# Kernel optimization log

Hardware: AMD Instinct MI355X
Metric: run time of the kernel (lower is better)

Reference implementation:

```python
import jax, jax.numpy as jnp
import numpy as np

N = 50000      # nodes
E = 800000     # edges
D_IN = 128
D_H = 128
D_OUT = 64
P = 0.3        # dropout prob


def _glorot(key, out_c, in_c):
    return jax.random.normal(key, (out_c, in_c), jnp.float32) * (1.0 / np.sqrt(in_c))


def setup_inputs() -> dict:
    key = jax.random.key(0)
    ks = jax.random.split(key, 10)
    return {
        "x": jax.random.normal(ks[0], (N, D_IN), jnp.float32),
        "u1": jax.random.uniform(ks[1], (N, D_H), jnp.float32),
        "u2": jax.random.uniform(ks[2], (N, D_H), jnp.float32),
        "wl0": _glorot(ks[3], D_H, D_IN), "bl0": jnp.zeros((D_H,), jnp.float32), "wr0": _glorot(ks[4], D_H, D_IN),
        "wl1": _glorot(ks[5], D_H, D_H), "bl1": jnp.zeros((D_H,), jnp.float32), "wr1": _glorot(ks[6], D_H, D_H),
        "wl2": _glorot(ks[7], D_OUT, D_H), "bl2": jnp.zeros((D_OUT,), jnp.float32), "wr2": _glorot(ks[8], D_OUT, D_H),
        "edge_index": jax.random.randint(ks[9], (2, E), 0, N),
    }


def _sage_conv(x, src, dst, wl, bl, wr):
    # PyG SAGEConv (aggr='mean'): lin_l(mean of neighbor msgs) + lin_r(x)
    msg = x[src]                                                    # [E, d] gather
    s = jax.ops.segment_sum(msg, dst, num_segments=N)               # [N, d] scatter-sum
    cnt = jax.ops.segment_sum(jnp.ones((dst.shape[0],), x.dtype), dst, num_segments=N)
    mean = s / jnp.maximum(cnt, 1.0)[:, None]                       # mean; 0 for isolated nodes
    return mean @ wl.T + bl + x @ wr.T


def reference(x, u1, u2, wl0, bl0, wr0, wl1, bl1, wr1, wl2, bl2, wr2, edge_index):
    src, dst = edge_index[0], edge_index[1]
    keep = 1.0 - P
    h = jax.nn.relu(_sage_conv(x, src, dst, wl0, bl0, wr0))
    h = h * ((u1 >= P).astype(h.dtype) / keep)                      # dropout (training=True)
    h = jax.nn.relu(_sage_conv(h, src, dst, wl1, bl1, wr1))
    h = h * ((u2 >= P).astype(h.dtype) / keep)
    return _sage_conv(h, src, dst, wl2, bl2, wr2)
```

## Files before the change

### kernel.cpp

```cpp
#include <hip/hip_runtime.h>


constexpr int N = 50000;
constexpr int E = 800000;
constexpr int NBUCK = (N + 255) / 256;
constexpr int CE = 2048;
constexpr int NEB = (E + CE - 1) / CE;
constexpr int SLOT = 5632;
static_assert(N <= 65536, "u16 packing");

typedef _Float16 f16x8 __attribute__((ext_vector_type(8)));
typedef _Float16 f16x4 __attribute__((ext_vector_type(4)));
typedef _Float16 f16x2 __attribute__((ext_vector_type(2)));
typedef float f32x4 __attribute__((ext_vector_type(4)));


__global__ __launch_bounds__(256) void bucket_scatter_kernel(
    const int* __restrict__ src, const int* __restrict__ dst,
    int* __restrict__ bcur, unsigned* __restrict__ T) {
  __shared__ unsigned sorted[CE];
  __shared__ int hist[256], scan[256], excl[256], lcur[256], gbase[256];
  const int t = threadIdx.x;
  const int e0 = blockIdx.x * CE;
  const int nval = min(CE, E - e0);
  hist[t] = 0;
  __syncthreads();
  for (int i = t; i < nval; i += 256) atomicAdd(&hist[dst[e0 + i] >> 8], 1);
  __syncthreads();
  const int h = hist[t];
  scan[t] = h;
  __syncthreads();
  for (int off = 1; off < 256; off <<= 1) {
    int u = (t >= off) ? scan[t - off] : 0;
    __syncthreads();
    scan[t] += u;
    __syncthreads();
  }
  excl[t] = scan[t] - h;
  lcur[t] = scan[t] - h;
  gbase[t] = (t < NBUCK && h > 0) ? atomicAdd(&bcur[t], h) : 0;
  __syncthreads();
  for (int i = t; i < nval; i += 256) {
    int e = e0 + i;
    int d = dst[e];
    int p = atomicAdd(&lcur[d >> 8], 1);
    sorted[p] = ((unsigned)d << 16) | (unsigned)src[e];
  }
  __syncthreads();
  for (int i = t; i < nval; i += 256) {
    unsigned pk = sorted[i];
    int b = pk >> 24;
    T[gbase[b] + (i - excl[b])] = pk;
  }
}

__global__ __launch_bounds__(256) void bucket_place_kernel(
    const unsigned* __restrict__ T, const int* __restrict__ bcur,
    int* __restrict__ offs, int* __restrict__ deg, int* __restrict__ elist) {
  __shared__ int dcnt[256], s[256], ncur[256];
  const int t = threadIdx.x;
  const int b = blockIdx.x;
  const int lo = b * SLOT;
  const int hi = bcur[b];
  dcnt[t] = 0;
  __syncthreads();
  for (int i = lo + t; i < hi; i += 256) atomicAdd(&dcnt[(T[i] >> 16) & 255], 1);
  __syncthreads();
  const int v = dcnt[t];
  const int pv = (v + 3) & ~3;
  s[t] = pv;
  __syncthreads();
  for (int off = 1; off < 256; off <<= 1) {
    int u = (t >= off) ? s[t - off] : 0;
    __syncthreads();
    s[t] += u;
    __syncthreads();
  }
  const int base = lo + s[t] - pv;
  const int node = b * 256 + t;
  if (node < N) { offs[node] = base; deg[node] = v; }
  ncur[t] = base;
  __syncthreads();
  for (int i = lo + t; i < hi; i += 256) {
    unsigned pk = T[i];
    int pos = atomicAdd(&ncur[(pk >> 16) & 255], 1);
    elist[pos] = (int)(pk & 0xffffu);
  }
}

__device__ inline void wfrag_build(int idx, int KB, const float* wl,
                                   const float* wr, _Float16* wf) {
  int j = idx & 7;
  int lane = (idx >> 3) & 63;
  int kb = (idx >> 9) % KB;
  int ct = (idx >> 9) / KB;
  int c = ct * 16 + (lane & 15);
  int k = kb * 32 + (lane >> 4) * 8 + j;
  float v = (k < 128) ? wl[c * 128 + k] : wr[c * 128 + (k - 128)];
  wf[idx] = (_Float16)v;
}

constexpr int CONVB = (N * 128 / 8 + 255) / 256;
constexpr int MASKB = (N * 128) / (8 * 256);

__global__ __launch_bounds__(256) void setup_kernel(
    const float* __restrict__ x,
    const float* __restrict__ u1, const float* __restrict__ u2,
    const float* __restrict__ wl0, const float* __restrict__ wr0,
    const float* __restrict__ wl1, const float* __restrict__ wr1,
    const float* __restrict__ wl2, const float* __restrict__ wr2,
    _Float16* __restrict__ HA, _Float16* __restrict__ wf0,
    _Float16* __restrict__ wf1, _Float16* __restrict__ wfZ,
    unsigned* __restrict__ mk1, unsigned* __restrict__ mk2,
    int* __restrict__ bcur) {
  const int b = blockIdx.x;
  const int t = threadIdx.x;
  if (b < CONVB) {
    int i = b * 256 + t;
    if (i < N * 128 / 8) {
      float4 a = ((const float4*)x)[i * 2];
      float4 c = ((const float4*)x)[i * 2 + 1];
      f16x8 v;
      v[0] = (_Float16)a.x; v[1] = (_Float16)a.y; v[2] = (_Float16)a.z; v[3] = (_Float16)a.w;
      v[4] = (_Float16)c.x; v[5] = (_Float16)c.y; v[6] = (_Float16)c.z; v[7] = (_Float16)c.w;
      ((f16x8*)HA)[i] = v;
    }
  } else if (b < CONVB + 128) {
    wfrag_build((b - CONVB) * 256 + t, 8, wl0, wr0, wf0);
  } else if (b < CONVB + 256) {
    wfrag_build((b - CONVB - 128) * 256 + t, 8, wl1, wr1, wf1);
  } else if (b < CONVB + 320) {
    int idx = (b - CONVB - 256) * 256 + t;
    int j = idx & 7;
    int lane = (idx >> 3) & 63;
    int kb = (idx >> 9) & 3;
    int ct = idx >> 11;
    int c = ct * 16 + (lane & 15);
    int k = kb * 32 + (lane >> 4) * 8 + j;
    float v = (c < 64) ? wl2[c * 128 + k] : wr2[(c - 64) * 128 + k];
    wfZ[idx] = (_Float16)v;
  } else if (b < CONVB + 320 + 2 * MASKB) {
    int mb = b - (CONVB + 320);
    const float* Us = (mb < MASKB) ? u1 : u2;
    unsigned* MKs = (mb < MASKB) ? mk1 : mk2;
    int bb = (mb < MASKB) ? mb : (mb - MASKB);
#pragma unroll
    for (int k = 0; k < 8; ++k) {
      int i = (bb * 8 + k) * 256 + t;
      float uv = Us[i];
      unsigned long long m = __ballot(uv >= 0.3f);
      int lt = t & 63;
      if (lt == 0) MKs[i >> 5] = (unsigned)m;
      else if (lt == 32) MKs[i >> 5] = (unsigned)(m >> 32);
    }
  } else {
    if (t < NBUCK) bcur[t] = t * SLOT;
  }
}

__global__ __launch_bounds__(256, 4) void fused_layer_kernel(
    const _Float16* __restrict__ H, const int* __restrict__ offs,
    const int* __restrict__ deg, const int* __restrict__ elist,
    const _Float16* __restrict__ Wf, const float* __restrict__ bias,
    const unsigned* __restrict__ MK, _Float16* __restrict__ outp) {
  __shared__ __align__(16) _Float16 Af[2][8][64][8];
  const int t = threadIdx.x;
  const int rowbase = blockIdx.x * 32;

#pragma unroll
  for (int m2 = 0; m2 < 2; ++m2) {
    int m = t * 2 + m2;
    int r = m >> 4, o = m & 15;
    int row = min(rowbase + r, N - 1);
    f16x8 v = *(const f16x8*)(H + (size_t)row * 128 + o * 8);
    *(f16x8*)&Af[r >> 4][4 + (o >> 2)][(o & 3) * 16 + (r & 15)][0] = v;
  }

  {
    const int hw = t >> 5;
    const int ll = t & 31;
    const int kb = ll >> 3, q = (ll >> 1) & 3, j = (ll & 1) * 4;
#pragma unroll 1
    for (int i = 0; i < 4; ++i) {
      int r = hw * 4 + i;
      int node = rowbase + r;
      float a0 = 0.f, a1 = 0.f, a2 = 0.f, a3 = 0.f;
      int d = 0;
      if (node < N) {
        const int e0 = offs[node];
        d = deg[node];
        const int e1 = e0 + d;
        int e = e0;
        for (; e + 16 <= e1; e += 16) {
          int4 q0 = *(const int4*)(elist + e);
          int4 q1 = *(const int4*)(elist + e + 4);
          int4 q2 = *(const int4*)(elist + e + 8);
          int4 q3 = *(const int4*)(elist + e + 12);
          int s[16] = {q0.x, q0.y, q0.z, q0.w, q1.x, q1.y, q1.z, q1.w,
                       q2.x, q2.y, q2.z, q2.w, q3.x, q3.y, q3.z, q3.w};
          f16x4 v[16];
#pragma unroll
          for (int u = 0; u < 16; ++u)
            v[u] = *(const f16x4*)(H + (size_t)s[u] * 128 + ll * 4);
#pragma unroll
          for (int u = 0; u < 16; ++u) {
            a0 += (float)v[u][0]; a1 += (float)v[u][1];
            a2 += (float)v[u][2]; a3 += (float)v[u][3];
          }
        }
        for (; e + 4 <= e1; e += 4) {
          int4 qq4 = *(const int4*)(elist + e);
          int s[4] = {qq4.x, qq4.y, qq4.z, qq4.w};
          f16x4 v[4];
#pragma unroll
          for (int u = 0; u < 4; ++u)
            v[u] = *(const f16x4*)(H + (size_t)s[u] * 128 + ll * 4);
#pragma unroll
          for (int u = 0; u < 4; ++u) {
            a0 += (float)v[u][0]; a1 += (float)v[u][1];
            a2 += (float)v[u][2]; a3 += (float)v[u][3];
          }
        }
        for (; e < e1; ++e) {
          f16x4 v = *(const f16x4*)(H + (size_t)elist[e] * 128 + ll * 4);
          a0 += (float)v[0]; a1 += (float)v[1];
          a2 += (float)v[2]; a3 += (float)v[3];
        }
      }
      float inv = 1.0f / (float)max(d, 1);
      f16x4 o;
      o[0] = (_Float16)(a0 * inv); o[1] = (_Float16)(a1 * inv);
      o[2] = (_Float16)(a2 * inv); o[3] = (_Float16)(a3 * inv);
      *(f16x4*)&Af[r >> 4][kb][q * 16 + (r & 15)][j] = o;
    }
  }
  __syncthreads();

  const int lane = t & 63;
  const int w = t >> 6;
  const int n16 = lane & 15;
  const int qq = lane >> 4;
  const int colbase = w * 32;

  f32x4 acc[2][2];
#pragma unroll
  for (int h = 0; h < 2; ++h)
#pragma unroll
    for (int ct = 0; ct < 2; ++ct) acc[h][ct] = (f32x4){0.f, 0.f, 0.f, 0.f};

#pragma unroll
  for (int kb = 0; kb < 8; ++kb) {
    f16x8 a0 = *(const f16x8*)&Af[0][kb][lane][0];
    f16x8 a1 = *(const f16x8*)&Af[1][kb][lane][0];
#pragma unroll
    for (int ct = 0; ct < 2; ++ct) {
      const int ctg = w * 2 + ct;
      f16x8 b = *(const f16x8*)(Wf + ((size_t)(ctg * 8 + kb) * 64 + lane) * 8);
      acc[0][ct] = __builtin_amdgcn_mfma_f32_16x16x32_f16(a0, b, acc[0][ct], 0, 0, 0);
      acc[1][ct] = __builtin_amdgcn_mfma_f32_16x16x32_f16(a1, b, acc[1][ct], 0, 0, 0);
    }
  }

#pragma unroll
  for (int h = 0; h < 2; ++h) {
#pragma unroll
    for (int r = 0; r < 4; ++r) {
      int row = rowbase + h * 16 + qq * 4 + r;
      if (row < N) {
        unsigned mw = MK[(size_t)row * 4 + w];
#pragma unroll
        for (int ct = 0; ct < 2; ++ct) {
          const int col = colbase + ct * 16 + n16;
          float v = fmaxf(acc[h][ct][r] + bias[col], 0.f);
          v = ((mw >> (ct * 16 + n16)) & 1u) ? v * (1.0f / 0.7f) : 0.0f;
          outp[(size_t)row * 128 + col] = (_Float16)v;
        }
      }
    }
  }
}

__global__ __launch_bounds__(256) void gather64_add_kernel(
    const _Float16* __restrict__ Y2, const float* __restrict__ F,
    const int* __restrict__ offs, const int* __restrict__ deg,
    const int* __restrict__ elist, float* __restrict__ out) {
  int node = blockIdx.x * 8 + (threadIdx.x >> 5);
  if (node >= N) return;
  int l = threadIdx.x & 31;
  const int e0 = offs[node];
  const int d = deg[node];
  const int e1 = e0 + d;
  float a0 = 0.f, a1 = 0.f;
  int e = e0;
  for (; e + 16 <= e1; e += 16) {
    int4 q0 = *(const int4*)(elist + e);
    int4 q1 = *(const int4*)(elist + e + 4);
    int4 q2 = *(const int4*)(elist + e + 8);
    int4 q3 = *(const int4*)(elist + e + 12);
    int s[16] = {q0.x, q0.y, q0.z, q0.w, q1.x, q1.y, q1.z, q1.w,
                 q2.x, q2.y, q2.z, q2.w, q3.x, q3.y, q3.z, q3.w};
    f16x2 v[16];
#pragma unroll
    for (int u = 0; u < 16; ++u)
      v[u] = *(const f16x2*)(Y2 + (size_t)s[u] * 64 + l * 2);
#pragma unroll
    for (int u = 0; u < 16; ++u) { a0 += (float)v[u][0]; a1 += (float)v[u][1]; }
  }
  for (; e + 4 <= e1; e += 4) {
    int4 q = *(const int4*)(elist + e);
    int s[4] = {q.x, q.y, q.z, q.w};
    f16x2 v[4];
#pragma unroll
    for (int u = 0; u < 4; ++u)
      v[u] = *(const f16x2*)(Y2 + (size_t)s[u] * 64 + l * 2);
#pragma unroll
    for (int u = 0; u < 4; ++u) { a0 += (float)v[u][0]; a1 += (float)v[u][1]; }
  }
  for (; e < e1; ++e) {
    f16x2 v = *(const f16x2*)(Y2 + (size_t)elist[e] * 64 + l * 2);
    a0 += (float)v[0]; a1 += (float)v[1];
  }
  float inv = 1.0f / (float)max(d, 1);
  float2 f = ((const float2*)(F + (size_t)node * 64))[l];
  float2 o;
  o.x = f.x + a0 * inv;
  o.y = f.y + a1 * inv;
  ((float2*)(out + (size_t)node * 64))[l] = o;
}

__global__ __launch_bounds__(256, 4) void mfma_gemmZ_kernel(
    const _Float16* __restrict__ Hh, const _Float16* __restrict__ Wf,
    const float* __restrict__ bl2, _Float16* __restrict__ Y2,
    float* __restrict__ F) {
  const int lane = threadIdx.x & 63;
  const int w = threadIdx.x >> 6;
  const int n16 = lane & 15;
  const int q = lane >> 4;
  const int rowbase = blockIdx.x * 32;
  const int colbase = w * 32;

  f32x4 acc[2][2];
#pragma unroll
  for (int h = 0; h < 2; ++h)
#pragma unroll
    for (int ct = 0; ct < 2; ++ct) acc[h][ct] = (f32x4){0.f, 0.f, 0.f, 0.f};

  int ar0 = min(rowbase + n16, N - 1);
  int ar1 = min(rowbase + 16 + n16, N - 1);
  const _Float16* pH0 = Hh + (size_t)ar0 * 128 + q * 8;
  const _Float16* pH1 = Hh + (size_t)ar1 * 128 + q * 8;

#pragma unroll
  for (int kb = 0; kb < 4; ++kb) {
    const int ko = kb * 32;
    f16x8 a0 = *(const f16x8*)(pH0 + ko);
    f16x8 a1 = *(const f16x8*)(pH1 + ko);
#pragma unroll
    for (int ct = 0; ct < 2; ++ct) {
      const int ctg = w * 2 + ct;
      f16x8 b = *(const f16x8*)(Wf + ((size_t)(ctg * 4 + kb) * 64 + lane) * 8);
      acc[0][ct] = __builtin_amdgcn_mfma_f32_16x16x32_f16(a0, b, acc[0][ct], 0, 0, 0);
      acc[1][ct] = __builtin_amdgcn_mfma_f32_16x16x32_f16(a1, b, acc[1][ct], 0, 0, 0);
    }
  }

#pragma unroll
  for (int h = 0; h < 2; ++h) {
#pragma unroll
    for (int ct = 0; ct < 2; ++ct) {
      const int col = colbase + ct * 16 + n16;
#pragma unroll
      for (int r = 0; r < 4; ++r) {
        int row = rowbase + h * 16 + q * 4 + r;
        if (row < N) {
          float v = acc[h][ct][r];
          if (col < 64) Y2[(size_t)row * 64 + col] = (_Float16)v;
          else F[(size_t)row * 64 + (col - 64)] = v + bl2[col - 64];
        }
      }
    }
  }
}

extern "C" void kernel_launch(void* const* d_in, const int* in_sizes, int n_in,
                              void* d_out, int out_size, void* d_ws, size_t ws_size,
                              hipStream_t stream) {
  const float* x   = (const float*)d_in[0];
  const float* u1  = (const float*)d_in[1];
  const float* u2  = (const float*)d_in[2];
  const float* wl0 = (const float*)d_in[3];
  const float* bl0 = (const float*)d_in[4];
  const float* wr0 = (const float*)d_in[5];
  const float* wl1 = (const float*)d_in[6];
  const float* bl1 = (const float*)d_in[7];
  const float* wr1 = (const float*)d_in[8];
  const float* wl2 = (const float*)d_in[9];
  const float* bl2 = (const float*)d_in[10];
  const float* wr2 = (const float*)d_in[11];
  const int* edge  = (const int*)d_in[12];
  const int* src = edge;
  const int* dst = edge + E;

  _Float16* HA  = (_Float16*)d_ws;
  _Float16* HB  = HA + (size_t)N * 128;
  _Float16* M16 = HB + (size_t)N * 128;
  float* F      = (float*)(M16 + (size_t)N * 128);
  int* offs     = (int*)(F + (size_t)N * 64);
  int* deg      = offs + N;
  int* elist    = deg + N;
  unsigned* T   = (unsigned*)(elist + NBUCK * SLOT);
  int* bcur     = (int*)(T + NBUCK * SLOT);
  uintptr_t p = (uintptr_t)(bcur + NBUCK);
  p = (p + 15) & ~(uintptr_t)15;
  _Float16* wf0 = (_Float16*)p;
  _Float16* wf1 = wf0 + 8 * 8 * 512;
  _Float16* wfZ = wf1 + 8 * 8 * 512;
  unsigned* mk1 = (unsigned*)(wfZ + 8 * 4 * 512);
  unsigned* mk2 = mk1 + (size_t)N * 4;

  setup_kernel<<<CONVB + 320 + 2 * MASKB + 1, 256, 0, stream>>>(
      x, u1, u2, wl0, wr0, wl1, wr1, wl2, wr2, HA, wf0, wf1, wfZ, mk1, mk2,
      bcur);
  bucket_scatter_kernel<<<NEB, 256, 0, stream>>>(src, dst, bcur, T);
  bucket_place_kernel<<<NBUCK, 256, 0, stream>>>(T, bcur, offs, deg, elist);

  const int GM   = (N + 31) / 32;
  const int GG64 = (N + 7) / 8;

  fused_layer_kernel<<<GM, 256, 0, stream>>>(HA, offs, deg, elist, wf0, bl0, mk1, HB);
  fused_layer_kernel<<<GM, 256, 0, stream>>>(HB, offs, deg, elist, wf1, bl1, mk2, HA);
  mfma_gemmZ_kernel<<<GM, 256, 0, stream>>>(HA, wfZ, bl2, M16, F);
  gather64_add_kernel<<<GG64, 256, 0, stream>>>(M16, F, offs, deg, elist,
                                                (float*)d_out);
}
```

Baseline: 314.2 us.

## Halve fused layer tile to 16 rows and move mask build into place kernel

After: 280.5 us. 10.7% less time.

```diff
diff --git a/kernel.cpp b/kernel.cpp
--- a/kernel.cpp
+++ b/kernel.cpp
@@ -8,6 +8,7 @@
 constexpr int NEB = (E + CE - 1) / CE;
 constexpr int SLOT = 5632;
 static_assert(N <= 65536, "u16 packing");
+static_assert(N % 16 == 0, "16-row blocks need no bounds checks");
 
 typedef _Float16 f16x8 __attribute__((ext_vector_type(8)));
 typedef _Float16 f16x4 __attribute__((ext_vector_type(4)));
@@ -54,12 +55,31 @@
   }
 }
 
+constexpr int MASKB = (N * 128) / (8 * 256);
+
 __global__ __launch_bounds__(256) void bucket_place_kernel(
     const unsigned* __restrict__ T, const int* __restrict__ bcur,
+    const float* __restrict__ u1, const float* __restrict__ u2,
+    unsigned* __restrict__ mk1, unsigned* __restrict__ mk2,
     int* __restrict__ offs, int* __restrict__ deg, int* __restrict__ elist) {
   __shared__ int dcnt[256], s[256], ncur[256];
   const int t = threadIdx.x;
   const int b = blockIdx.x;
+  if (b >= NBUCK) {
+    int mb = b - NBUCK;
+    const float* Us = (mb < MASKB) ? u1 : u2;
+    unsigned* MKs = (mb < MASKB) ? mk1 : mk2;
+    int bb = (mb < MASKB) ? mb : (mb - MASKB);
+#pragma unroll
+    for (int k = 0; k < 8; ++k) {
+      int i = (bb * 8 + k) * 256 + t;
+      unsigned long long m = __ballot(Us[i] >= 0.3f);
+      int lt = t & 63;
+      if (lt == 0) MKs[i >> 5] = (unsigned)m;
+      else if (lt == 32) MKs[i >> 5] = (unsigned)(m >> 32);
+    }
+    return;
+  }
   const int lo = b * SLOT;
   const int hi = bcur[b];
   dcnt[t] = 0;
@@ -101,17 +121,14 @@
 }
 
 constexpr int CONVB = (N * 128 / 8 + 255) / 256;
-constexpr int MASKB = (N * 128) / (8 * 256);
 
 __global__ __launch_bounds__(256) void setup_kernel(
     const float* __restrict__ x,
-    const float* __restrict__ u1, const float* __restrict__ u2,
     const float* __restrict__ wl0, const float* __restrict__ wr0,
     const float* __restrict__ wl1, const float* __restrict__ wr1,
     const float* __restrict__ wl2, const float* __restrict__ wr2,
     _Float16* __restrict__ HA, _Float16* __restrict__ wf0,
     _Float16* __restrict__ wf1, _Float16* __restrict__ wfZ,
-    unsigned* __restrict__ mk1, unsigned* __restrict__ mk2,
     int* __restrict__ bcur) {
   const int b = blockIdx.x;
   const int t = threadIdx.x;
@@ -139,41 +156,24 @@
     int k = kb * 32 + (lane >> 4) * 8 + j;
     float v = (c < 64) ? wl2[c * 128 + k] : wr2[(c - 64) * 128 + k];
     wfZ[idx] = (_Float16)v;
-  } else if (b < CONVB + 320 + 2 * MASKB) {
-    int mb = b - (CONVB + 320);
-    const float* Us = (mb < MASKB) ? u1 : u2;
-    unsigned* MKs = (mb < MASKB) ? mk1 : mk2;
-    int bb = (mb < MASKB) ? mb : (mb - MASKB);
-#pragma unroll
-    for (int k = 0; k < 8; ++k) {
-      int i = (bb * 8 + k) * 256 + t;
-      float uv = Us[i];
-      unsigned long long m = __ballot(uv >= 0.3f);
-      int lt = t & 63;
-      if (lt == 0) MKs[i >> 5] = (unsigned)m;
-      else if (lt == 32) MKs[i >> 5] = (unsigned)(m >> 32);
-    }
   } else {
     if (t < NBUCK) bcur[t] = t * SLOT;
   }
 }
 
-__global__ __launch_bounds__(256, 4) void fused_layer_kernel(
+__global__ __launch_bounds__(256, 8) void fused_layer_kernel(
     const _Float16* __restrict__ H, const int* __restrict__ offs,
     const int* __restrict__ deg, const int* __restrict__ elist,
     const _Float16* __restrict__ Wf, const float* __restrict__ bias,
     const unsigned* __restrict__ MK, _Float16* __restrict__ outp) {
-  __shared__ __align__(16) _Float16 Af[2][8][64][8];
+  __shared__ __align__(16) _Float16 Af[8][64][8];
   const int t = threadIdx.x;
-  const int rowbase = blockIdx.x * 32;
-
-#pragma unroll
-  for (int m2 = 0; m2 < 2; ++m2) {
-    int m = t * 2 + m2;
-    int r = m >> 4, o = m & 15;
-    int row = min(rowbase + r, N - 1);
-    f16x8 v = *(const f16x8*)(H + (size_t)row * 128 + o * 8);
-    *(f16x8*)&Af[r >> 4][4 + (o >> 2)][(o & 3) * 16 + (r & 15)][0] = v;
+  const int rowbase = blockIdx.x * 16;
+
+  {
+    int r = t >> 4, o = t & 15;
+    f16x8 v = *(const f16x8*)(H + (size_t)(rowbase + r) * 128 + o * 8);
+    *(f16x8*)&Af[4 + (o >> 2)][(o & 3) * 16 + r][0] = v;
   }
 
   {
@@ -181,57 +181,54 @@
     const int ll = t & 31;
     const int kb = ll >> 3, q = (ll >> 1) & 3, j = (ll & 1) * 4;
 #pragma unroll 1
-    for (int i = 0; i < 4; ++i) {
-      int r = hw * 4 + i;
+    for (int i = 0; i < 2; ++i) {
+      int r = hw * 2 + i;
       int node = rowbase + r;
       float a0 = 0.f, a1 = 0.f, a2 = 0.f, a3 = 0.f;
-      int d = 0;
-      if (node < N) {
-        const int e0 = offs[node];
-        d = deg[node];
-        const int e1 = e0 + d;
-        int e = e0;
-        for (; e + 16 <= e1; e += 16) {
-          int4 q0 = *(const int4*)(elist + e);
-          int4 q1 = *(const int4*)(elist + e + 4);
-          int4 q2 = *(const int4*)(elist + e + 8);
-          int4 q3 = *(const int4*)(elist + e + 12);
-          int s[16] = {q0.x, q0.y, q0.z, q0.w, q1.x, q1.y, q1.z, q1.w,
-                       q2.x, q2.y, q2.z, q2.w, q3.x, q3.y, q3.z, q3.w};
-          f16x4 v[16];
-#pragma unroll
-          for (int u = 0; u < 16; ++u)
-            v[u] = *(const f16x4*)(H + (size_t)s[u] * 128 + ll * 4);
-#pragma unroll
-          for (int u = 0; u < 16; ++u) {
-            a0 += (float)v[u][0]; a1 += (float)v[u][1];
-            a2 += (float)v[u][2]; a3 += (float)v[u][3];
-          }
+      const int e0 = offs[node];
+      const int d = deg[node];
+      const int e1 = e0 + d;
+      int e = e0;
+      for (; e + 16 <= e1; e += 16) {
+        int4 q0 = *(const int4*)(elist + e);
+        int4 q1 = *(const int4*)(elist + e + 4);
+        int4 q2 = *(const int4*)(elist + e + 8);
+        int4 q3 = *(const int4*)(elist + e + 12);
+        int s[16] = {q0.x, q0.y, q0.z, q0.w, q1.x, q1.y, q1.z, q1.w,
+                     q2.x, q2.y, q2.z, q2.w, q3.x, q3.y, q3.z, q3.w};
+        f16x4 v[16];
+#pragma unroll
+        for (int u = 0; u < 16; ++u)
+          v[u] = *(const f16x4*)(H + (size_t)s[u] * 128 + ll * 4);
+#pragma unroll
+        for (int u = 0; u < 16; ++u) {
+          a0 += (float)v[u][0]; a1 += (float)v[u][1];
+          a2 += (float)v[u][2]; a3 += (float)v[u][3];
         }
-        for (; e + 4 <= e1; e += 4) {
-          int4 qq4 = *(const int4*)(elist + e);
-          int s[4] = {qq4.x, qq4.y, qq4.z, qq4.w};
-          f16x4 v[4];
-#pragma unroll
-          for (int u = 0; u < 4; ++u)
-            v[u] = *(const f16x4*)(H + (size_t)s[u] * 128 + ll * 4);
-#pragma unroll
-          for (int u = 0; u < 4; ++u) {
-            a0 += (float)v[u][0]; a1 += (float)v[u][1];
-            a2 += (float)v[u][2]; a3 += (float)v[u][3];
-          }
+      }
+      for (; e + 4 <= e1; e += 4) {
+        int4 qq4 = *(const int4*)(elist + e);
+        int s[4] = {qq4.x, qq4.y, qq4.z, qq4.w};
+        f16x4 v[4];
+#pragma unroll
+        for (int u = 0; u < 4; ++u)
+          v[u] = *(const f16x4*)(H + (size_t)s[u] * 128 + ll * 4);
+#pragma unroll
+        for (int u = 0; u < 4; ++u) {
+          a0 += (float)v[u][0]; a1 += (float)v[u][1];
+          a2 += (float)v[u][2]; a3 += (float)v[u][3];
         }
-        for (; e < e1; ++e) {
-          f16x4 v = *(const f16x4*)(H + (size_t)elist[e] * 128 + ll * 4);
-          a0 += (float)v[0]; a1 += (float)v[1];
-          a2 += (float)v[2]; a3 += (float)v[3];
-        }
+      }
+      for (; e < e1; ++e) {
+        f16x4 v = *(const f16x4*)(H + (size_t)elist[e] * 128 + ll * 4);
+        a0 += (float)v[0]; a1 += (float)v[1];
+        a2 += (float)v[2]; a3 += (float)v[3];
       }
       float inv = 1.0f / (float)max(d, 1);
       f16x4 o;
       o[0] = (_Float16)(a0 * inv); o[1] = (_Float16)(a1 * inv);
       o[2] = (_Float16)(a2 * inv); o[3] = (_Float16)(a3 * inv);
-      *(f16x4*)&Af[r >> 4][kb][q * 16 + (r & 15)][j] = o;
+      *(f16x4*)&Af[kb][q * 16 + r][j] = o;
     }
   }
   __syncthreads();
@@ -242,40 +239,31 @@
   const int qq = lane >> 4;
   const int colbase = w * 32;
 
-  f32x4 acc[2][2];
-#pragma unroll
-  for (int h = 0; h < 2; ++h)
-#pragma unroll
-    for (int ct = 0; ct < 2; ++ct) acc[h][ct] = (f32x4){0.f, 0.f, 0.f, 0.f};
+  f32x4 acc[2];
+  acc[0] = (f32x4){0.f, 0.f, 0.f, 0.f};
+  acc[1] = (f32x4){0.f, 0.f, 0.f, 0.f};
 
 #pragma unroll
   for (int kb = 0; kb < 8; ++kb) {
-    f16x8 a0 = *(const f16x8*)&Af[0][kb][lane][0];
-    f16x8 a1 = *(const f16x8*)&Af[1][kb][lane][0];
+    f16x8 a = *(const f16x8*)&Af[kb][lane][0];
 #pragma unroll
     for (int ct = 0; ct < 2; ++ct) {
       const int ctg = w * 2 + ct;
       f16x8 b = *(const f16x8*)(Wf + ((size_t)(ctg * 8 + kb) * 64 + lane) * 8);
-      acc[0][ct] = __builtin_amdgcn_mfma_f32_16x16x32_f16(a0, b, acc[0][ct], 0, 0, 0);
-      acc[1][ct] = __builtin_amdgcn_mfma_f32_16x16x32_f16(a1, b, acc[1][ct], 0, 0, 0);
-    }
-  }
-
-#pragma unroll
-  for (int h = 0; h < 2; ++h) {
-#pragma unroll
-    for (int r = 0; r < 4; ++r) {
-      int row = rowbase + h * 16 + qq * 4 + r;
-      if (row < N) {
-        unsigned mw = MK[(size_t)row * 4 + w];
-#pragma unroll
-        for (int ct = 0; ct < 2; ++ct) {
-          const int col = colbase + ct * 16 + n16;
-          float v = fmaxf(acc[h][ct][r] + bias[col], 0.f);
-          v = ((mw >> (ct * 16 + n16)) & 1u) ? v * (1.0f / 0.7f) : 0.0f;
-          outp[(size_t)row * 128 + col] = (_Float16)v;
-        }
-      }
+      acc[ct] = __builtin_amdgcn_mfma_f32_16x16x32_f16(a, b, acc[ct], 0, 0, 0);
+    }
+  }
+
+#pragma unroll
+  for (int r = 0; r < 4; ++r) {
+    int row = rowbase + qq * 4 + r;
+    unsigned mw = MK[(size_t)row * 4 + w];
+#pragma unroll
+    for (int ct = 0; ct < 2; ++ct) {
+      const int col = colbase + ct * 16 + n16;
+      float v = fmaxf(acc[ct][r] + bias[col], 0.f);
+      v = ((mw >> (ct * 16 + n16)) & 1u) ? v * (1.0f / 0.7f) : 0.0f;
+      outp[(size_t)row * 128 + col] = (_Float16)v;
     }
   }
 }
@@ -418,17 +406,18 @@
   unsigned* mk1 = (unsigned*)(wfZ + 8 * 4 * 512);
   unsigned* mk2 = mk1 + (size_t)N * 4;
 
-  setup_kernel<<<CONVB + 320 + 2 * MASKB + 1, 256, 0, stream>>>(
-      x, u1, u2, wl0, wr0, wl1, wr1, wl2, wr2, HA, wf0, wf1, wfZ, mk1, mk2,
-      bcur);
+  setup_kernel<<<CONVB + 321, 256, 0, stream>>>(
+      x, wl0, wr0, wl1, wr1, wl2, wr2, HA, wf0, wf1, wfZ, bcur);
   bucket_scatter_kernel<<<NEB, 256, 0, stream>>>(src, dst, bcur, T);
-  bucket_place_kernel<<<NBUCK, 256, 0, stream>>>(T, bcur, offs, deg, elist);
-
+  bucket_place_kernel<<<NBUCK + 2 * MASKB, 256, 0, stream>>>(
+      T, bcur, u1, u2, mk1, mk2, offs, deg, elist);
+
+  const int GM16 = N / 16;
   const int GM   = (N + 31) / 32;
   const int GG64 = (N + 7) / 8;
 
-  fused_layer_kernel<<<GM, 256, 0, stream>>>(HA, offs, deg, elist, wf0, bl0, mk1, HB);
-  fused_layer_kernel<<<GM, 256, 0, stream>>>(HB, offs, deg, elist, wf1, bl1, mk2, HA);
+  fused_layer_kernel<<<GM16, 256, 0, stream>>>(HA, offs, deg, elist, wf0, bl0, mk1, HB);
+  fused_layer_kernel<<<GM16, 256, 0, stream>>>(HB, offs, deg, elist, wf1, bl1, mk2, HA);
   mfma_gemmZ_kernel<<<GM, 256, 0, stream>>>(HA, wfZ, bl2, M16, F);
   gather64_add_kernel<<<GG64, 256, 0, stream>>>(M16, F, offs, deg, elist,
                                                 (float*)d_out);
```
